# Kernel tuning notes

Hardware: AMD Instinct MI355X
Metric: run time of the kernel (lower is better)

Reference implementation:

```python
import math
import jax, jax.numpy as jnp
import numpy as np
from jax import lax

SAMPLE_RATE = 16000
BLOCK_SIZE = 64
B = 524288


def setup_inputs() -> dict:
    key = jax.random.key(0)
    k1, k2, k3 = jax.random.split(key, 3)
    fm_params = jax.random.uniform(k1, (B, 1, 6), dtype=jnp.float32)
    # realistic fundamentals in [50, 400) Hz; module clamps to >=1 anyway
    f0_hz = 50.0 + 350.0 * jax.random.uniform(k2, (B, 1), dtype=jnp.float32)
    phase_state = jax.random.uniform(k3, (B, 4), dtype=jnp.float32)
    return {"fm_params": fm_params, "f0_hz": f0_hz, "phase_state": phase_state}


def reference(fm_params, f0_hz, phase_state):
    # T == 1 (module requirement), so squeeze the frame dim everywhere.
    dtype = fm_params.dtype
    two_pi = 2.0 * math.pi

    f0 = jnp.clip(f0_hz[:, 0], 1.0, None)            # [B]
    p = fm_params[:, 0, :]                            # [B, 6]
    # parameter mappings (op1 mod depth p[:,0] is unused, as in the original)
    r1 = 0.25 + p[:, 1] * 15.75
    fb1 = p[:, 2] * 0.95
    d2 = p[:, 3] * 10.0
    r2 = 0.25 + p[:, 4] * 15.75
    fb2 = p[:, 5] * 0.95

    inc1 = two_pi * f0 * r1 / SAMPLE_RATE             # [B]
    inc2 = two_pi * f0 * r2 / SAMPLE_RATE

    start1 = phase_state[:, 0]                        # frame start phases
    start2 = phase_state[:, 1]
    last1_0 = phase_state[:, 2]                       # feedback buffers
    last2_0 = phase_state[:, 3]

    offsets = jnp.arange(BLOCK_SIZE, dtype=dtype)     # [S]
    # per-sample phases, scanned over the sample axis: [S, B]
    phase1 = start1[None, :] + offsets[:, None] * inc1[None, :]
    phase2 = start2[None, :] + offsets[:, None] * inc2[None, :]

    def step(carry, ph):
        l1, l2 = carry
        ph1, ph2 = ph
        o1 = jnp.sin(ph1 + fb1 * l1)                  # op1 with self-feedback
        o2 = jnp.sin(ph2 + d2 * o1 + fb2 * l2)        # op2 carrier, FM'd by op1
        return (o1, o2), o2

    (l1f, l2f), samples = lax.scan(step, (last1_0, last2_0), (phase1, phase2))
    audio = samples.T                                 # [B, S]

    rms = jnp.sqrt(jnp.mean(audio * audio, axis=-1, keepdims=True) + 1e-5)
    audio = audio / rms

    phase_end = jnp.stack(
        [
            (start1 + BLOCK_SIZE * inc1) % two_pi,
            (start2 + BLOCK_SIZE * inc2) % two_pi,
            l1f,
            l2f,
        ],
        axis=-1,
    )                                                 # [B, 4]
    return audio, phase_end
```

## Files before the change

### kernel.cpp

```cpp
#include <hip/hip_runtime.h>

#define NBLOCK 64

__device__ __forceinline__ float fast_sinf(float x) {
    float kf = rintf(x * 0.63661977236758134f);
    int   q  = (int)kf;
    float r = fmaf(kf, -1.5707963705062866f, x);
    r = fmaf(kf, 4.3711390001862171e-8f, r);
    float z = r * r;
    float s = fmaf(z, fmaf(z, -1.9515295891e-4f, 8.3321608736e-3f), -1.6666654611e-1f);
    float sinr = fmaf(z * r, s, r);
    float c = fmaf(z, fmaf(z, 2.4433157118e-5f, -1.3887316255e-3f), 4.1666645683e-2f);
    float cosr = fmaf(z, fmaf(z, c, -0.5f), 1.0f);
    float res = (q & 1) ? cosr : sinr;
    return (q & 2) ? -res : res;
}

__device__ __forceinline__ float mod_two_pi(float x) {
    const float Y = 6.2831853071795864769f;
    float kf = floorf(__fdiv_rn(x, Y));
    float m = fmaf(-kf, Y, x);
    if (m < 0.0f)  { kf -= 1.0f; m = fmaf(-kf, Y, x); }
    if (m >= Y)    { kf += 1.0f; m = fmaf(-kf, Y, x); }
    return m;
}

__global__ __launch_bounds__(256)
void fm_synth_kernel(const float* __restrict__ fm_params,
                     const float* __restrict__ f0_hz,
                     const float* __restrict__ phase_state,
                     float* __restrict__ out, int nv)
{
    __shared__ float lds[256 * 17];

    int tid = threadIdx.x;
    int b   = blockIdx.x * 256 + tid;
    int bc  = min(b, nv - 1);
    bool live = (b < nv);

    const float2* fm2 = (const float2*)fm_params;
    float2 p01 = fm2[bc * 3 + 0];
    float2 p23 = fm2[bc * 3 + 1];
    float2 p45 = fm2[bc * 3 + 2];
    float  f0  = fmaxf(f0_hz[bc], 1.0f);
    float4 st  = ((const float4*)phase_state)[bc];

    const float TWO_PI = 6.2831853071795864769f;
    float r1  = __fadd_rn(0.25f, __fmul_rn(p01.y, 15.75f));
    float fb1 = __fmul_rn(p23.x, 0.95f);
    float d2  = __fmul_rn(p23.y, 10.0f);
    float r2  = __fadd_rn(0.25f, __fmul_rn(p45.x, 15.75f));
    float fb2 = __fmul_rn(p45.y, 0.95f);
    float inc1 = __fdiv_rn(__fmul_rn(__fmul_rn(TWO_PI, f0), r1), 16000.0f);
    float inc2 = __fdiv_rn(__fmul_rn(__fmul_rn(TWO_PI, f0), r2), 16000.0f);

    float start1 = st.x, start2 = st.y;
    float l1 = st.z, l2 = st.w;

    float smp[NBLOCK];
#pragma unroll
    for (int t = 0; t < NBLOCK; ++t) {
        float tf  = (float)t;
        float ph1 = tf * inc1 + start1;
        float ph2 = tf * inc2 + start2;
        float o1 = fast_sinf(ph1 + fb1 * l1);
        float o2 = fast_sinf(ph2 + d2 * o1 + fb2 * l2);
        l1 = o1;
        l2 = o2;
        smp[t] = o2;
    }

    float ss = 0.0f;
#pragma unroll
    for (int t = 0; t < NBLOCK; ++t) ss = fmaf(smp[t], smp[t], ss);
    float inv = 1.0f / sqrtf(ss * 0.015625f + 1e-5f);
#pragma unroll
    for (int t = 0; t < NBLOCK; ++t) smp[t] *= inv;

    float4* out4 = (float4*)out;
    int blockBase = blockIdx.x * 256;
    int u  = tid & 3;
    int v0 = tid >> 2;
#pragma unroll
    for (int c = 0; c < 4; ++c) {
        __syncthreads();
        float* slot = &lds[tid * 17];
#pragma unroll
        for (int i = 0; i < 16; ++i) slot[i] = smp[c * 16 + i];
        __syncthreads();
#pragma unroll
        for (int k = 0; k < 4; ++k) {
            int v = v0 + 64 * k;
            const float* src = &lds[v * 17 + u * 4];
            float4 val;
            val.x = src[0]; val.y = src[1]; val.z = src[2]; val.w = src[3];
            if (blockBase + v < nv)
                out4[(size_t)(blockBase + v) * 16 + 4 * c + u] = val;
        }
    }

    float x1 = __fadd_rn(start1, __fmul_rn(64.0f, inc1));
    float x2 = __fadd_rn(start2, __fmul_rn(64.0f, inc2));
    float4 pe;
    pe.x = mod_two_pi(x1);
    pe.y = mod_two_pi(x2);
    pe.z = l1;
    pe.w = l2;
    if (live)
        ((float4*)(out + (size_t)nv * NBLOCK))[b] = pe;
}

extern "C" void kernel_launch(void* const* d_in, const int* in_sizes, int n_in,
                              void* d_out, int out_size, void* d_ws, size_t ws_size,
                              hipStream_t stream) {
    const float* fm_params   = (const float*)d_in[0];
    const float* f0_hz       = (const float*)d_in[1];
    const float* phase_state = (const float*)d_in[2];
    float* out = (float*)d_out;
    int nv = in_sizes[1];
    int grid = (nv + 255) / 256;
    fm_synth_kernel<<<grid, 256, 0, stream>>>(fm_params, f0_hz, phase_state, out, nv);
}
```

Before: 171.2 us.

## Use grid-stride persistent blocks and fully coalesced float4 output staging via LDS

The kernel becomes persistent, running at most 512 blocks that loop over voices with a grid stride. The LDS transpose now stages 128 voices at a time in two halves, written with float4 stores at a padded stride of 68. Each wave then writes contiguous global float4 runs rather than 4-wide chunks scattered across voices. The goal is more coalesced output writes and lower launch and tail costs. In exchange, each half of the block idles while the other half writes to LDS, and 512 blocks may not fill all CUs on MI355X with enough waves to hide latency.

```diff
diff --git a/kernel.cpp b/kernel.cpp
--- a/kernel.cpp
+++ b/kernel.cpp
@@ -1,6 +1,10 @@
 #include <hip/hip_runtime.h>
 
 #define NBLOCK 64
+#define TPB 256
+#define SUBV 128
+#define LDSTR 68
+#define MAXGRID 512
 
 __device__ __forceinline__ float fast_sinf(float x) {
     float kf = rintf(x * 0.63661977236758134f);
@@ -25,89 +29,101 @@
     return m;
 }
 
-__global__ __launch_bounds__(256)
+__global__ __launch_bounds__(TPB)
 void fm_synth_kernel(const float* __restrict__ fm_params,
                      const float* __restrict__ f0_hz,
                      const float* __restrict__ phase_state,
                      float* __restrict__ out, int nv)
 {
-    __shared__ float lds[256 * 17];
+    __shared__ float lds[SUBV * LDSTR];
 
-    int tid = threadIdx.x;
-    int b   = blockIdx.x * 256 + tid;
-    int bc  = min(b, nv - 1);
-    bool live = (b < nv);
+    const int tid    = threadIdx.x;
+    const int stride = gridDim.x * TPB;
+    float4* out4 = (float4*)out;
+    float4* pe4  = (float4*)(out + (size_t)nv * NBLOCK);
 
-    const float2* fm2 = (const float2*)fm_params;
-    float2 p01 = fm2[bc * 3 + 0];
-    float2 p23 = fm2[bc * 3 + 1];
-    float2 p45 = fm2[bc * 3 + 2];
-    float  f0  = fmaxf(f0_hz[bc], 1.0f);
-    float4 st  = ((const float4*)phase_state)[bc];
+    for (int base = blockIdx.x * TPB; base < nv; base += stride) {
+        int  b    = base + tid;
+        int  bc   = min(b, nv - 1);
+        bool live = (b < nv);
 
-    const float TWO_PI = 6.2831853071795864769f;
-    float r1  = __fadd_rn(0.25f, __fmul_rn(p01.y, 15.75f));
-    float fb1 = __fmul_rn(p23.x, 0.95f);
-    float d2  = __fmul_rn(p23.y, 10.0f);
-    float r2  = __fadd_rn(0.25f, __fmul_rn(p45.x, 15.75f));
-    float fb2 = __fmul_rn(p45.y, 0.95f);
-    float inc1 = __fdiv_rn(__fmul_rn(__fmul_rn(TWO_PI, f0), r1), 16000.0f);
-    float inc2 = __fdiv_rn(__fmul_rn(__fmul_rn(TWO_PI, f0), r2), 16000.0f);
+        const float2* fm2 = (const float2*)fm_params;
+        float2 p01 = fm2[bc * 3 + 0];
+        float2 p23 = fm2[bc * 3 + 1];
+        float2 p45 = fm2[bc * 3 + 2];
+        float  f0  = fmaxf(f0_hz[bc], 1.0f);
+        float4 st  = ((const float4*)phase_state)[bc];
 
-    float start1 = st.x, start2 = st.y;
-    float l1 = st.z, l2 = st.w;
+        const float TWO_PI = 6.2831853071795864769f;
+        float r1  = __fadd_rn(0.25f, __fmul_rn(p01.y, 15.75f));
+        float fb1 = __fmul_rn(p23.x, 0.95f);
+        float d2  = __fmul_rn(p23.y, 10.0f);
+        float r2  = __fadd_rn(0.25f, __fmul_rn(p45.x, 15.75f));
+        float fb2 = __fmul_rn(p45.y, 0.95f);
+        float inc1 = __fdiv_rn(__fmul_rn(__fmul_rn(TWO_PI, f0), r1), 16000.0f);
+        float inc2 = __fdiv_rn(__fmul_rn(__fmul_rn(TWO_PI, f0), r2), 16000.0f);
 
-    float smp[NBLOCK];
+        float start1 = st.x, start2 = st.y;
+        float l1 = st.z, l2 = st.w;
+
+        float smp[NBLOCK];
 #pragma unroll
-    for (int t = 0; t < NBLOCK; ++t) {
-        float tf  = (float)t;
-        float ph1 = tf * inc1 + start1;
-        float ph2 = tf * inc2 + start2;
-        float o1 = fast_sinf(ph1 + fb1 * l1);
-        float o2 = fast_sinf(ph2 + d2 * o1 + fb2 * l2);
-        l1 = o1;
-        l2 = o2;
-        smp[t] = o2;
-    }
+        for (int t = 0; t < NBLOCK; ++t) {
+            float tf  = (float)t;
+            float ph1 = tf * inc1 + start1;
+            float ph2 = tf * inc2 + start2;
+            float o1 = fast_sinf(ph1 + fb1 * l1);
+            float o2 = fast_sinf(ph2 + d2 * o1 + fb2 * l2);
+            l1 = o1;
+            l2 = o2;
+            smp[t] = o2;
+        }
 
-    float ss = 0.0f;
+        float ss = 0.0f;
 #pragma unroll
-    for (int t = 0; t < NBLOCK; ++t) ss = fmaf(smp[t], smp[t], ss);
-    float inv = 1.0f / sqrtf(ss * 0.015625f + 1e-5f);
+        for (int t = 0; t < NBLOCK; ++t) ss = fmaf(smp[t], smp[t], ss);
+        float inv = 1.0f / sqrtf(ss * 0.015625f + 1e-5f);
 #pragma unroll
-    for (int t = 0; t < NBLOCK; ++t) smp[t] *= inv;
+        for (int t = 0; t < NBLOCK; ++t) smp[t] *= inv;
 
-    float4* out4 = (float4*)out;
-    int blockBase = blockIdx.x * 256;
-    int u  = tid & 3;
-    int v0 = tid >> 2;
+        float x1 = __fadd_rn(start1, __fmul_rn(64.0f, inc1));
+        float x2 = __fadd_rn(start2, __fmul_rn(64.0f, inc2));
+        float4 pe;
+        pe.x = mod_two_pi(x1);
+        pe.y = mod_two_pi(x2);
+        pe.z = l1;
+        pe.w = l2;
+        if (live) pe4[b] = pe;
+
+        int halfw = tid >> 7;
+        int vi    = tid & (SUBV - 1);
 #pragma unroll
-    for (int c = 0; c < 4; ++c) {
-        __syncthreads();
-        float* slot = &lds[tid * 17];
+        for (int s = 0; s < 2; ++s) {
+            __syncthreads();
+            if (halfw == s) {
+                float* slot = &lds[vi * LDSTR];
 #pragma unroll
-        for (int i = 0; i < 16; ++i) slot[i] = smp[c * 16 + i];
-        __syncthreads();
+                for (int i = 0; i < 16; ++i) {
+                    float4 v4;
+                    v4.x = smp[4 * i + 0];
+                    v4.y = smp[4 * i + 1];
+                    v4.z = smp[4 * i + 2];
+                    v4.w = smp[4 * i + 3];
+                    *(float4*)&slot[4 * i] = v4;
+                }
+            }
+            __syncthreads();
+            size_t gbase = (size_t)(base + s * SUBV) * 16;
 #pragma unroll
-        for (int k = 0; k < 4; ++k) {
-            int v = v0 + 64 * k;
-            const float* src = &lds[v * 17 + u * 4];
-            float4 val;
-            val.x = src[0]; val.y = src[1]; val.z = src[2]; val.w = src[3];
-            if (blockBase + v < nv)
-                out4[(size_t)(blockBase + v) * 16 + 4 * c + u] = val;
+            for (int j = 0; j < 8; ++j) {
+                int f    = j * TPB + tid;
+                int voff = f >> 4;
+                float4 val = *(const float4*)&lds[voff * LDSTR + 4 * (f & 15)];
+                if (base + s * SUBV + voff < nv)
+                    out4[gbase + f] = val;
+            }
         }
     }
-
-    float x1 = __fadd_rn(start1, __fmul_rn(64.0f, inc1));
-    float x2 = __fadd_rn(start2, __fmul_rn(64.0f, inc2));
-    float4 pe;
-    pe.x = mod_two_pi(x1);
-    pe.y = mod_two_pi(x2);
-    pe.z = l1;
-    pe.w = l2;
-    if (live)
-        ((float4*)(out + (size_t)nv * NBLOCK))[b] = pe;
 }
 
 extern "C" void kernel_launch(void* const* d_in, const int* in_sizes, int n_in,
@@ -118,6 +134,8 @@
     const float* phase_state = (const float*)d_in[2];
     float* out = (float*)d_out;
     int nv = in_sizes[1];
-    int grid = (nv + 255) / 256;
-    fm_synth_kernel<<<grid, 256, 0, stream>>>(fm_params, f0_hz, phase_state, out, nv);
+    int nblocks = (nv + TPB - 1) / TPB;
+    int grid = nblocks < MAXGRID ? nblocks : MAXGRID;
+    if (grid < 1) grid = 1;
+    fm_synth_kernel<<<grid, TPB, 0, stream>>>(fm_params, f0_hz, phase_state, out, nv);
 }
```

Result: slower. 182.4 us (+6.5%).
